# Kernel optimization log

Measured on AMD Instinct MI355X. Metric: run time of the kernel, lower is better.

## Reference

```python
import jax, jax.numpy as jnp
import numpy as np

N_NODES = 10000
N_EDGES = 160000
N_GRAPHS = 64
F = 80        # hidden dim
T = 5         # towers
F_OUT = 16    # per-tower post output (80/5)
N_LAYERS = 4
EPS = 1e-6
BN_EPS = 1e-5
STD_EPS = 1e-5


def setup_inputs() -> dict:
    key = jax.random.key(0)
    ks = jax.random.split(key, 12)
    x = jax.random.uniform(ks[0], (N_NODES, 2), dtype=jnp.float32)
    edge_index = jax.random.randint(ks[1], (2, N_EDGES), 0, N_NODES, dtype=jnp.int64)
    batch = jnp.sort(jax.random.randint(ks[2], (N_NODES,), 0, N_GRAPHS, dtype=jnp.int64))

    def w(k, shape, fan_in):
        return (jax.random.normal(k, shape, jnp.float32) / np.float32(np.sqrt(fan_in)))

    return {
        "x": x, "edge_index": edge_index, "batch": batch,
        "pre_lin_W": w(ks[3], (1, F), 1), "pre_lin_b": jnp.zeros((F,), jnp.float32),
        "pre_W": w(ks[4], (N_LAYERS, T, 2 * F, F), 2 * F), "pre_b": jnp.zeros((N_LAYERS, T, F), jnp.float32),
        "post_W": w(ks[5], (N_LAYERS, T, 13 * F, F_OUT), 13 * F), "post_b": jnp.zeros((N_LAYERS, T, F_OUT), jnp.float32),
        "lin_W": w(ks[6], (N_LAYERS, F, F), F), "lin_b": jnp.zeros((N_LAYERS, F), jnp.float32),
        "bn_gamma": jnp.ones((N_LAYERS, F), jnp.float32), "bn_beta": jnp.zeros((N_LAYERS, F), jnp.float32),
        "mlp_lin_W": w(ks[7], (40, 1), 40), "mlp_lin_b": jnp.zeros((1,), jnp.float32),
        "mlp1_W": w(ks[8], (40, 20), 40), "mlp1_b": jnp.zeros((20,), jnp.float32),
        "mlp2_W": w(ks[9], (20, 1), 20), "mlp2_b": jnp.zeros((1,), jnp.float32),
    }


def _pna_conv(h, src, dst, deg, avg_log_deg, preW, preb, postW, postb, linW, linb):
    # h: [N, F]; messages per tower: pre MLP over cat(x_i, x_j)  (divide_input=False)
    N = h.shape[0]
    hm = jnp.concatenate([h[dst], h[src]], axis=-1)            # [E, 2F]
    m = jnp.einsum('ef,tfo->eto', hm, preW) + preb             # [E, T, F]

    cnt = jnp.maximum(deg, 1.0)[:, None, None]                 # [N,1,1]
    has = (deg > 0)[:, None, None]
    s = jax.ops.segment_sum(m, dst, num_segments=N)
    mean = s / cnt
    mean_sq = jax.ops.segment_sum(m * m, dst, num_segments=N) / cnt
    mn = jax.ops.segment_min(m, dst, num_segments=N)
    mx = jax.ops.segment_max(m, dst, num_segments=N)
    mn = jnp.where(has, mn, 0.0)
    mx = jnp.where(has, mx, 0.0)
    std = jnp.sqrt(jax.nn.relu(mean_sq - mean * mean) + STD_EPS)
    agg = jnp.concatenate([mean, mn, mx, std], axis=-1)        # [N, T, 4F]

    logd = jnp.log(jnp.maximum(deg, 1.0) + 1.0)[:, None, None]
    amp = agg * (logd / avg_log_deg)
    att = agg * (avg_log_deg / logd)
    out = jnp.concatenate([agg, amp, att], axis=-1)            # [N, T, 12F]

    xt = jnp.broadcast_to(h[:, None, :], (N, T, F))
    out = jnp.concatenate([xt, out], axis=-1)                  # [N, T, 13F]
    out = jnp.einsum('ntf,tfo->nto', out, postW) + postb       # [N, T, F_OUT]
    out = out.reshape(N, T * F_OUT)                            # [N, 80]
    return out @ linW + linb


def _forward(x, edge_index, batch, pre_lin_W, pre_lin_b, pre_W, pre_b,
             post_W, post_b, lin_W, lin_b, bn_gamma, bn_beta,
             mlp_lin_W, mlp_lin_b, mlp1_W, mlp1_b, mlp2_W, mlp2_b):
    N = x.shape[0]
    src, dst = edge_index[0], edge_index[1]
    deg = jax.ops.segment_sum(jnp.ones_like(dst, jnp.float32), dst, num_segments=N)
    avg_log_deg = jnp.mean(jnp.log(deg + 1.0))                 # PNA avg log-degree from deg histogram

    operation = x[:, 0:1]
    assignment = x[:, 1:2]
    op = operation @ pre_lin_W + pre_lin_b                     # [N, 80]

    for l in range(N_LAYERS):
        y = _pna_conv(op, src, dst, deg, avg_log_deg,
                      pre_W[l], pre_b[l], post_W[l], post_b[l], lin_W[l], lin_b[l])
        mu = jnp.mean(y, axis=0)
        var = jnp.mean((y - mu) ** 2, axis=0)                  # biased, training-mode BN
        y = (y - mu) / jnp.sqrt(var + BN_EPS) * bn_gamma[l] + bn_beta[l]
        op = jax.nn.relu(y)

    front, behind = op[:, :40], op[:, 40:]
    xc = front * assignment + behind                           # [N, 40], non-negative

    # LastLayer: log-space scatter-add message passing
    log_score = jax.ops.segment_sum(jnp.log(xc[src] + EPS), dst, num_segments=N)
    xc = jnp.exp(log_score + jnp.log(xc + EPS))

    # global mean pool over graphs
    gcnt = jnp.maximum(jax.ops.segment_sum(jnp.ones_like(batch, jnp.float32), batch, num_segments=N_GRAPHS), 1.0)
    pooled = jax.ops.segment_sum(xc, batch, num_segments=N_GRAPHS) / gcnt[:, None]  # [B, 40]

    x_lin = pooled @ mlp_lin_W + mlp_lin_b
    x_cv = pooled @ mlp1_W + mlp1_b
    x_cv = 20.0 - jax.nn.relu(x_cv)
    x_cv = x_cv @ mlp2_W + mlp2_b
    return x_cv + x_lin                                        # [B, 1]


def reference(x, edge_index, batch, pre_lin_W, pre_lin_b, pre_W, pre_b,
              post_W, post_b, lin_W, lin_b, bn_gamma, bn_beta,
              mlp_lin_W, mlp_lin_b, mlp1_W, mlp1_b, mlp2_W, mlp2_b):
    return _forward(x, edge_index, batch, pre_lin_W, pre_lin_b, pre_W, pre_b,
                    post_W, post_b, lin_W, lin_b, bn_gamma, bn_beta,
                    mlp_lin_W, mlp_lin_b, mlp1_W, mlp1_b, mlp2_W, mlp2_b)
```

## Files before the change

### kernel.cpp

```cpp
#include <hip/hip_runtime.h>
#include <math.h>

#define NN 10000
#define NE 160000
#define NG 64
#define FEAT 80
#define NT 5
#define NL 4

__global__ void k_cnt2(const int* __restrict__ dst, const int* __restrict__ batch,
                       int* __restrict__ deg, int* __restrict__ gcnt) {
    int e = blockIdx.x * 256 + threadIdx.x;
    if (e < NE) atomicAdd(&deg[dst[e]], 1);
    if (e < NN) atomicAdd(&gcnt[batch[e]], 1);
}

__global__ void k_scan(const int* __restrict__ deg, int* __restrict__ offs) {
    __shared__ int sums[256];
    int tid = threadIdx.x;
    int start = tid * 40, stop = min(start + 40, NN);
    int s = 0;
    for (int i = start; i < stop; ++i) s += deg[i];
    sums[tid] = s;
    __syncthreads();
    for (int off = 1; off < 256; off <<= 1) {
        int v = (tid >= off) ? sums[tid - off] : 0;
        __syncthreads();
        sums[tid] += v;
        __syncthreads();
    }
    int base = (tid == 0) ? 0 : sums[tid - 1];
    for (int i = start; i < stop; ++i) { offs[i] = base; base += deg[i]; }
    if (tid == 255) offs[NN] = sums[255];
}

__global__ void k_ald(const int* __restrict__ deg, float* __restrict__ ald) {
    __shared__ float red[256];
    int i = blockIdx.x * 256 + threadIdx.x;
    red[threadIdx.x] = (i < NN) ? logf((float)deg[i] + 1.0f) : 0.0f;
    __syncthreads();
    for (int s = 128; s > 0; s >>= 1) {
        if (threadIdx.x < s) red[threadIdx.x] += red[threadIdx.x + s];
        __syncthreads();
    }
    if (threadIdx.x == 0) atomicAdd(ald, red[0]);
}

__global__ void k_fill(const int* __restrict__ src, const int* __restrict__ dst,
                       const int* __restrict__ offs, int* __restrict__ cursor,
                       int* __restrict__ csr) {
    int e = blockIdx.x * 256 + threadIdx.x;
    if (e < NE) {
        int d = dst[e];
        int p = atomicAdd(&cursor[d], 1);
        csr[offs[d] + p] = src[e];
    }
}

__global__ void k_op0(const float* __restrict__ x, const float* __restrict__ plW,
                      const float* __restrict__ plb, float* __restrict__ hT) {
    int i = blockIdx.x * 256 + threadIdx.x;
    if (i < FEAT * NN) {
        int f = i / NN, n = i - f * NN;
        hT[i] = x[2 * n] * plW[f] + plb[f];
    }
}

__global__ __launch_bounds__(256) void k_mm_ab(
        const float* __restrict__ hT, const float* __restrict__ preW_l,
        float* __restrict__ A, float* __restrict__ Bt) {
    __shared__ float hs[16][80];
    int n0 = blockIdx.x * 16;
    int tid = threadIdx.x;
    for (int i = tid; i < 16 * 80; i += 256) {
        int nl = i & 15, f = i >> 4;
        hs[nl][f] = hT[(size_t)f * NN + n0 + nl];
    }
    __syncthreads();
    float acc[4][16];
#pragma unroll
    for (int s = 0; s < 4; s++)
#pragma unroll
        for (int i = 0; i < 16; i++) acc[s][i] = 0.f;
    const float* wp[4];
#pragma unroll
    for (int s = 0; s < 4; s++) {
        int c = tid + s * 256;
        int cs = (c < 800) ? c : 0;
        int part = (cs >= 400) ? 1 : 0;
        int cc = cs - part * 400;
        int t = cc / 80, o = cc - t * 80;
        wp[s] = preW_l + (size_t)(t * 160 + part * 80) * 80 + o;
    }
    for (int fq = 0; fq < 80; fq += 4) {
        float w[4][4];
#pragma unroll
        for (int s = 0; s < 4; s++) {
            w[s][0] = wp[s][(fq + 0) * 80];
            w[s][1] = wp[s][(fq + 1) * 80];
            w[s][2] = wp[s][(fq + 2) * 80];
            w[s][3] = wp[s][(fq + 3) * 80];
        }
#pragma unroll
        for (int i = 0; i < 16; i++) {
            float4 hv = *(const float4*)&hs[i][fq];
#pragma unroll
            for (int s = 0; s < 4; s++) {
                acc[s][i] += hv.x * w[s][0] + hv.y * w[s][1] +
                             hv.z * w[s][2] + hv.w * w[s][3];
            }
        }
    }
#pragma unroll
    for (int s = 0; s < 4; s++) {
        int c = tid + s * 256;
        if (c < 800) {
            int part = (c >= 400) ? 1 : 0;
            int cc = c - part * 400;
            int t = cc / 80, o = cc - t * 80;
            if (part == 0) {
#pragma unroll
                for (int i = 0; i < 16; i++) A[(size_t)(n0 + i) * 400 + cc] = acc[s][i];
            } else {
#pragma unroll
                for (int i = 0; i < 16; i++)
                    Bt[((size_t)t * NN + n0 + i) * 80 + o] = acc[s][i];
            }
        }
    }
}

__global__ __launch_bounds__(256) void k_agg_t(
        const float* __restrict__ A, const float* __restrict__ Bt,
        const int* __restrict__ offs, const int* __restrict__ csr,
        const float* __restrict__ preb_l, float* __restrict__ aggT) {
    __shared__ float st[320 * 17];
    int tid = threadIdx.x;
    int id = blockIdx.y * 625 + blockIdx.x;
    int xcd = id & 7;
    int slot = id >> 3;
    int base = (xcd <= 5) ? xcd * 391 : 5 * 391 + (xcd - 5) * 390;
    int r = base + slot;
    int t = r / 625;
    int n0 = (r - t * 625) * 16;
    int ni = tid >> 4;
    int cl = tid & 15;
    int n = n0 + ni;
    int e0 = offs[n], e1 = offs[n + 1];
    const float* Bts = Bt + (size_t)t * NN * 80;
    float s[5], q[5], mn[5], mx[5];
#pragma unroll
    for (int k = 0; k < 5; k++) { s[k] = 0.f; q[k] = 0.f; mn[k] = 3.4e38f; mx[k] = -3.4e38f; }
    int e = e0;
    for (; e + 3 < e1; e += 4) {
        const float* br0 = Bts + (size_t)csr[e] * 80 + cl;
        const float* br1 = Bts + (size_t)csr[e + 1] * 80 + cl;
        const float* br2 = Bts + (size_t)csr[e + 2] * 80 + cl;
        const float* br3 = Bts + (size_t)csr[e + 3] * 80 + cl;
#pragma unroll
        for (int k = 0; k < 5; k++) {
            float b0 = br0[k * 16];
            float b1 = br1[k * 16];
            float b2 = br2[k * 16];
            float b3 = br3[k * 16];
            s[k] += (b0 + b1) + (b2 + b3);
            q[k] += (b0 * b0 + b1 * b1) + (b2 * b2 + b3 * b3);
            mn[k] = fminf(mn[k], fminf(fminf(b0, b1), fminf(b2, b3)));
            mx[k] = fmaxf(mx[k], fmaxf(fmaxf(b0, b1), fmaxf(b2, b3)));
        }
    }
    for (; e < e1; ++e) {
        const float* br = Bts + (size_t)csr[e] * 80 + cl;
#pragma unroll
        for (int k = 0; k < 5; k++) {
            float b = br[k * 16];
            s[k] += b; q[k] += b * b;
            mn[k] = fminf(mn[k], b); mx[k] = fmaxf(mx[k], b);
        }
    }
    int d = e1 - e0;
    float degf = (float)d;
    float cnt = fmaxf(degf, 1.f);
#pragma unroll
    for (int k = 0; k < 5; k++) {
        int c = cl + k * 16;
        float a = A[(size_t)n * 400 + t * 80 + c] + preb_l[t * 80 + c];
        float mean = (degf * a + s[k]) / cnt;
        float msq  = (degf * a * a + 2.f * a * s[k] + q[k]) / cnt;
        float sd = sqrtf(fmaxf(msq - mean * mean, 0.f) + 1e-5f);
        float mnr = (d > 0) ? a + mn[k] : 0.f;
        float mxr = (d > 0) ? a + mx[k] : 0.f;
        st[(0 * 80 + c) * 17 + ni] = mean;
        st[(1 * 80 + c) * 17 + ni] = mnr;
        st[(2 * 80 + c) * 17 + ni] = mxr;
        st[(3 * 80 + c) * 17 + ni] = sd;
    }
    __syncthreads();
    int jj = tid >> 4;
    int nl = tid & 15;
#pragma unroll
    for (int pass = 0; pass < 20; ++pass) {
        int j = pass * 16 + jj;
        aggT[((size_t)t * 320 + j) * NN + n0 + nl] = st[j * 17 + nl];
    }
}

__global__ __launch_bounds__(256) void k_post(
        const float* __restrict__ hT, const float* __restrict__ aggT,
        const float* __restrict__ postW_l, const float* __restrict__ postb_l,
        const int* __restrict__ offs, const float* __restrict__ ald_sum,
        float* __restrict__ y0T) {
    __shared__ float wj[40 * 48];
    __shared__ float wh[80 * 16];
    int tid = threadIdx.x;
    int t = blockIdx.y;
    int jq = blockIdx.z;
    int j0 = jq * 40;
    const float* W0 = postW_l + (size_t)t * 1040 * 16;
    const float* W1 = W0 + 80 * 16;
    const float* W2 = W0 + 400 * 16;
    const float* W3 = W0 + 720 * 16;
    for (int idx = tid; idx < 40 * 48; idx += 256) {
        int j = idx / 48;
        int rem = idx - j * 48;
        int p = rem >> 4, o = rem & 15;
        const float* Wp = (p == 0) ? W1 : (p == 1) ? W2 : W3;
        wj[idx] = Wp[(j0 + j) * 16 + o];
    }
    if (jq == 0) {
        for (int idx = tid; idx < 80 * 16; idx += 256)
            wh[idx] = W0[idx];
    }
    __syncthreads();
    int n = blockIdx.x * 256 + tid;
    bool alive = (n < NN);
    int nc = alive ? n : 0;
    float acc1[16], acc2[16], acc3[16];
#pragma unroll
    for (int i = 0; i < 16; i++) { acc1[i] = 0.f; acc2[i] = 0.f; acc3[i] = 0.f; }
    const float* ap = aggT + ((size_t)t * 320 + j0) * NN + nc;
#pragma unroll 8
    for (int j = 0; j < 40; ++j) {
        float a = ap[(size_t)j * NN];
        const float* w = wj + j * 48;
#pragma unroll
        for (int i = 0; i < 16; i++) {
            acc1[i] += a * w[i];
            acc2[i] += a * w[16 + i];
            acc3[i] += a * w[32 + i];
        }
    }
    if (jq == 0) {
#pragma unroll 4
        for (int f = 0; f < 80; ++f) {
            float hv = hT[(size_t)f * NN + nc];
            const float* w = wh + f * 16;
#pragma unroll
            for (int i = 0; i < 16; i++) acc1[i] += hv * w[i];
        }
    }
    if (alive) {
        float degf = (float)(offs[n + 1] - offs[n]);
        float ald = ald_sum[0] * (1.f / NN);
        float logd = logf(fmaxf(degf, 1.f) + 1.f);
        float c1 = logd / ald;
        float c2 = ald / logd;
#pragma unroll
        for (int i = 0; i < 16; i++) {
            float v = acc1[i] + c1 * acc2[i] + c2 * acc3[i];
            if (jq == 0) v += postb_l[t * 16 + i];
            unsafeAtomicAdd(&y0T[(size_t)(t * 16 + i) * NN + n], v);
        }
    }
}

__global__ __launch_bounds__(256) void k_lin(
        const float* __restrict__ y0T, const float* __restrict__ linW_l,
        const float* __restrict__ linb_l, float* __restrict__ yT) {
    __shared__ float ws[80 * 8];
    int tid = threadIdx.x;
    int f0 = blockIdx.y * 8;
    for (int idx = tid; idx < 80 * 8; idx += 256)
        ws[idx] = linW_l[(idx >> 3) * 80 + f0 + (idx & 7)];
    __syncthreads();
    int n = blockIdx.x * 256 + tid;
    bool alive = (n < NN);
    int nc = alive ? n : 0;
    float acc[8];
#pragma unroll
    for (int i = 0; i < 8; i++) acc[i] = 0.f;
#pragma unroll 8
    for (int k = 0; k < 80; ++k) {
        float v = y0T[(size_t)k * NN + nc];
        const float4 wa = *(const float4*)(ws + k * 8);
        const float4 wb = *(const float4*)(ws + k * 8 + 4);
        acc[0] += v * wa.x; acc[1] += v * wa.y; acc[2] += v * wa.z; acc[3] += v * wa.w;
        acc[4] += v * wb.x; acc[5] += v * wb.y; acc[6] += v * wb.z; acc[7] += v * wb.w;
    }
    if (alive) {
#pragma unroll
        for (int i = 0; i < 8; i++)
            yT[(size_t)(f0 + i) * NN + n] = acc[i] + linb_l[f0 + i];
    }
}

__global__ void k_bnstats(const float* __restrict__ yT, float* __restrict__ bnst) {
    __shared__ float r1[256], r2[256];
    int f = blockIdx.x;
    int seg = blockIdx.y;
    int tid = threadIdx.x;
    int i0 = seg * 1250, i1 = min(i0 + 1250, NN);
    float s = 0.f, q = 0.f;
    for (int i = i0 + tid; i < i1; i += 256) {
        float v = yT[(size_t)f * NN + i];
        s += v; q += v * v;
    }
    r1[tid] = s; r2[tid] = q;
    __syncthreads();
    for (int st = 128; st > 0; st >>= 1) {
        if (tid < st) { r1[tid] += r1[tid + st]; r2[tid] += r2[tid + st]; }
        __syncthreads();
    }
    if (tid == 0) {
        unsafeAtomicAdd(&bnst[f], r1[0]);
        unsafeAtomicAdd(&bnst[80 + f], r2[0]);
    }
}

__global__ void k_bn(const float* __restrict__ yT, const float* __restrict__ bnst,
                     const float* __restrict__ gamma_l, const float* __restrict__ beta_l,
                     float* __restrict__ hT) {
    int i = blockIdx.x * 256 + threadIdx.x;
    if (i >= FEAT * NN) return;
    int f = i / NN;
    float mu = bnst[f] * (1.f / NN);
    float msq = bnst[80 + f] * (1.f / NN);
    float var = fmaxf(msq - mu * mu, 0.f);
    float v = (yT[i] - mu) * (1.f / sqrtf(var + 1e-5f)) * gamma_l[f] + beta_l[f];
    hT[i] = fmaxf(v, 0.f);
}

__global__ void k_bnxc(const float* __restrict__ yT, const float* __restrict__ bnst,
                       const float* __restrict__ gamma_l, const float* __restrict__ beta_l,
                       const float* __restrict__ x, float* __restrict__ lxc) {
    int i = blockIdx.x * 256 + threadIdx.x;
    if (i >= 40 * NN) return;
    int f = i / NN, n = i - f * NN;
    int f2 = f + 40;
    float mu1 = bnst[f] * (1.f / NN);
    float ms1 = bnst[80 + f] * (1.f / NN);
    float v1 = (yT[(size_t)f * NN + n] - mu1) *
               (1.f / sqrtf(fmaxf(ms1 - mu1 * mu1, 0.f) + 1e-5f)) * gamma_l[f] + beta_l[f];
    v1 = fmaxf(v1, 0.f);
    float mu2 = bnst[f2] * (1.f / NN);
    float ms2 = bnst[80 + f2] * (1.f / NN);
    float v2 = (yT[(size_t)f2 * NN + n] - mu2) *
               (1.f / sqrtf(fmaxf(ms2 - mu2 * mu2, 0.f) + 1e-5f)) * gamma_l[f2] + beta_l[f2];
    v2 = fmaxf(v2, 0.f);
    lxc[(size_t)n * 40 + f] = logf(v1 * x[2 * n + 1] + v2 + 1e-6f);
}

__global__ void k_logagg(const float* __restrict__ lxc, const int* __restrict__ offs,
                         const int* __restrict__ csr, const int* __restrict__ batch,
                         float* __restrict__ pooled) {
    int n = blockIdx.x;
    int tid = threadIdx.x;
    if (tid >= 40) return;
    int e0 = offs[n], e1 = offs[n + 1];
    float s = 0.f;
    for (int k = e0; k < e1; ++k) s += lxc[(size_t)csr[k] * 40 + tid];
    float v = expf(s + lxc[(size_t)n * 40 + tid]);
    atomicAdd(&pooled[batch[n] * 40 + tid], v);
}

__global__ void k_final(const float* __restrict__ pooled, const int* __restrict__ gcnt,
                        const float* __restrict__ mlW, const float* __restrict__ mlb,
                        const float* __restrict__ m1W, const float* __restrict__ m1b,
                        const float* __restrict__ m2W, const float* __restrict__ m2b,
                        float* __restrict__ out) {
    int g = threadIdx.x;
    if (g >= NG) return;
    float inv = 1.f / fmaxf((float)gcnt[g], 1.f);
    float pl[40];
#pragma unroll
    for (int j = 0; j < 40; j++) pl[j] = pooled[g * 40 + j] * inv;
    float xl = mlb[0];
#pragma unroll
    for (int j = 0; j < 40; j++) xl += pl[j] * mlW[j];
    float acc = m2b[0];
    for (int k = 0; k < 20; k++) {
        float v = m1b[k];
#pragma unroll
        for (int j = 0; j < 40; j++) v += pl[j] * m1W[j * 20 + k];
        v = 20.f - fmaxf(v, 0.f);
        acc += v * m2W[k];
    }
    out[g] = acc + xl;
}

extern "C" void kernel_launch(void* const* d_in, const int* in_sizes, int n_in,
                              void* d_out, int out_size, void* d_ws, size_t ws_size,
                              hipStream_t stream) {
    const float* x     = (const float*)d_in[0];
    const int*   ei    = (const int*)d_in[1];
    const int*   batch = (const int*)d_in[2];
    const float* plW   = (const float*)d_in[3];
    const float* plb   = (const float*)d_in[4];
    const float* preW  = (const float*)d_in[5];
    const float* preb  = (const float*)d_in[6];
    const float* postW = (const float*)d_in[7];
    const float* postb = (const float*)d_in[8];
    const float* linW  = (const float*)d_in[9];
    const float* linb  = (const float*)d_in[10];
    const float* bnG   = (const float*)d_in[11];
    const float* bnB   = (const float*)d_in[12];
    const float* mlW   = (const float*)d_in[13];
    const float* mlb   = (const float*)d_in[14];
    const float* m1W   = (const float*)d_in[15];
    const float* m1b   = (const float*)d_in[16];
    const float* m2W   = (const float*)d_in[17];
    const float* m2b   = (const float*)d_in[18];
    float* out = (float*)d_out;
    const int* srcp = ei;
    const int* dstp = ei + NE;

    char* p = (char*)d_ws;
    int*   deg    = (int*)(p + 0);
    int*   cursor = (int*)(p + 40000);
    int*   gcnt   = (int*)(p + 80000);
    float* ald    = (float*)(p + 80256);
    float* pooled = (float*)(p + 80272);
    float* bnst   = (float*)(p + 90512);
    int*   offs   = (int*)(p + 93072);
    int*   csr    = (int*)(p + 133088);
    float* hT     = (float*)(p + 773088);
    float* A      = (float*)(p + 3973088);
    float* Bt     = (float*)(p + 19973088);
    float* aggT   = (float*)(p + 35973088);
    float* y0T = (float*)(p + 23173088);
    float* yT  = (float*)(p + 26373088);
    float* lxc = (float*)(p + 35973088);

    hipMemsetAsync(d_ws, 0, 93072, stream);
    k_cnt2<<<dim3((NE + 255) / 256), 256, 0, stream>>>(dstp, batch, deg, gcnt);
    k_scan<<<1, 256, 0, stream>>>(deg, offs);
    k_ald<<<dim3((NN + 255) / 256), 256, 0, stream>>>(deg, ald);
    k_fill<<<dim3((NE + 255) / 256), 256, 0, stream>>>(srcp, dstp, offs, cursor, csr);
    k_op0<<<dim3((FEAT * NN + 255) / 256), 256, 0, stream>>>(x, plW, plb, hT);

    for (int l = 0; l < NL; ++l) {
        const float* preW_l  = preW  + (size_t)l * NT * 160 * 80;
        const float* preb_l  = preb  + l * NT * 80;
        const float* postW_l = postW + (size_t)l * NT * 1040 * 16;
        const float* postb_l = postb + l * NT * 16;
        const float* linW_l  = linW  + l * 80 * 80;
        const float* linb_l  = linb  + l * 80;
        float* bnst_l = bnst + l * 160;
        k_mm_ab<<<dim3(625), 256, 0, stream>>>(hT, preW_l, A, Bt);
        k_agg_t<<<dim3(625, 5), 256, 0, stream>>>(A, Bt, offs, csr, preb_l, aggT);
        hipMemsetAsync(y0T, 0, (size_t)80 * NN * 4, stream);
        k_post<<<dim3(40, 5, 8), 256, 0, stream>>>(hT, aggT, postW_l, postb_l, offs, ald, y0T);
        k_lin<<<dim3(40, 10), 256, 0, stream>>>(y0T, linW_l, linb_l, yT);
        k_bnstats<<<dim3(80, 8), 256, 0, stream>>>(yT, bnst_l);
        if (l < NL - 1) {
            k_bn<<<dim3((FEAT * NN + 255) / 256), 256, 0, stream>>>(
                yT, bnst_l, bnG + l * 80, bnB + l * 80, hT);
        } else {
            k_bnxc<<<dim3((40 * NN + 255) / 256), 256, 0, stream>>>(
                yT, bnst_l, bnG + l * 80, bnB + l * 80, x, lxc);
        }
    }

    k_logagg<<<dim3(NN), 64, 0, stream>>>(lxc, offs, csr, batch, pooled);
    k_final<<<1, 64, 0, stream>>>(pooled, gcnt, mlW, mlb, m1W, m1b, m2W, m2b, out);
}
```

Baseline: 781.5 us.

## Fuse PNA aggregation and post-tower projection into one kernel

Merges the aggregation kernel with the post MLP. Each 16-node tower tile now multiplies its shared-memory statistics directly by the post weights, with a split-K shared-memory reduction across four thread groups. This removes the round trip of the large aggT buffer through global memory, the memset of y0T, and the atomic accumulation. In exchange, weights are read from global or cache per block rather than staged in LDS, and the reduction adds extra syncs and leaves most threads idle during the final step.

```diff
diff --git a/kernel.cpp b/kernel.cpp
--- a/kernel.cpp
+++ b/kernel.cpp
@@ -130,10 +130,12 @@
     }
 }
 
-__global__ __launch_bounds__(256) void k_agg_t(
+__global__ __launch_bounds__(256) void k_aggpost(
         const float* __restrict__ A, const float* __restrict__ Bt,
         const int* __restrict__ offs, const int* __restrict__ csr,
-        const float* __restrict__ preb_l, float* __restrict__ aggT) {
+        const float* __restrict__ preb_l, const float* __restrict__ hT,
+        const float* __restrict__ postW_l, const float* __restrict__ postb_l,
+        const float* __restrict__ ald_sum, float* __restrict__ y0T) {
     __shared__ float st[320 * 17];
     int tid = threadIdx.x;
     int id = blockIdx.y * 625 + blockIdx.x;
@@ -196,80 +198,64 @@
         st[(3 * 80 + c) * 17 + ni] = sd;
     }
     __syncthreads();
-    int jj = tid >> 4;
-    int nl = tid & 15;
-#pragma unroll
-    for (int pass = 0; pass < 20; ++pass) {
-        int j = pass * 16 + jj;
-        aggT[((size_t)t * 320 + j) * NN + n0 + nl] = st[j * 17 + nl];
-    }
-}
-
-__global__ __launch_bounds__(256) void k_post(
-        const float* __restrict__ hT, const float* __restrict__ aggT,
-        const float* __restrict__ postW_l, const float* __restrict__ postb_l,
-        const int* __restrict__ offs, const float* __restrict__ ald_sum,
-        float* __restrict__ y0T) {
-    __shared__ float wj[40 * 48];
-    __shared__ float wh[80 * 16];
-    int tid = threadIdx.x;
-    int t = blockIdx.y;
-    int jq = blockIdx.z;
-    int j0 = jq * 40;
+    int ni2 = tid & 15;
+    int og  = (tid >> 4) & 3;
+    int js  = tid >> 6;
     const float* W0 = postW_l + (size_t)t * 1040 * 16;
-    const float* W1 = W0 + 80 * 16;
-    const float* W2 = W0 + 400 * 16;
-    const float* W3 = W0 + 720 * 16;
-    for (int idx = tid; idx < 40 * 48; idx += 256) {
-        int j = idx / 48;
-        int rem = idx - j * 48;
-        int p = rem >> 4, o = rem & 15;
-        const float* Wp = (p == 0) ? W1 : (p == 1) ? W2 : W3;
-        wj[idx] = Wp[(j0 + j) * 16 + o];
-    }
-    if (jq == 0) {
-        for (int idx = tid; idx < 80 * 16; idx += 256)
-            wh[idx] = W0[idx];
-    }
-    __syncthreads();
-    int n = blockIdx.x * 256 + tid;
-    bool alive = (n < NN);
-    int nc = alive ? n : 0;
-    float acc1[16], acc2[16], acc3[16];
-#pragma unroll
-    for (int i = 0; i < 16; i++) { acc1[i] = 0.f; acc2[i] = 0.f; acc3[i] = 0.f; }
-    const float* ap = aggT + ((size_t)t * 320 + j0) * NN + nc;
-#pragma unroll 8
-    for (int j = 0; j < 40; ++j) {
-        float a = ap[(size_t)j * NN];
-        const float* w = wj + j * 48;
-#pragma unroll
-        for (int i = 0; i < 16; i++) {
-            acc1[i] += a * w[i];
-            acc2[i] += a * w[16 + i];
-            acc3[i] += a * w[32 + i];
-        }
-    }
-    if (jq == 0) {
-#pragma unroll 4
-        for (int f = 0; f < 80; ++f) {
-            float hv = hT[(size_t)f * NN + nc];
-            const float* w = wh + f * 16;
-#pragma unroll
-            for (int i = 0; i < 16; i++) acc1[i] += hv * w[i];
-        }
-    }
-    if (alive) {
-        float degf = (float)(offs[n + 1] - offs[n]);
+    float a1[4], a2[4], a3[4];
+#pragma unroll
+    for (int i = 0; i < 4; i++) { a1[i] = 0.f; a2[i] = 0.f; a3[i] = 0.f; }
+    int jb = js * 80;
+#pragma unroll 2
+    for (int j = jb; j < jb + 80; ++j) {
+        float a = st[j * 17 + ni2];
+        float4 w1 = *(const float4*)(W0 + (size_t)(80 + j) * 16 + og * 4);
+        float4 w2 = *(const float4*)(W0 + (size_t)(400 + j) * 16 + og * 4);
+        float4 w3 = *(const float4*)(W0 + (size_t)(720 + j) * 16 + og * 4);
+        a1[0] += a * w1.x; a1[1] += a * w1.y; a1[2] += a * w1.z; a1[3] += a * w1.w;
+        a2[0] += a * w2.x; a2[1] += a * w2.y; a2[2] += a * w2.z; a2[3] += a * w2.w;
+        a3[0] += a * w3.x; a3[1] += a * w3.y; a3[2] += a * w3.z; a3[3] += a * w3.w;
+    }
+    int fb = js * 20;
+#pragma unroll 2
+    for (int f = fb; f < fb + 20; ++f) {
+        float hv = hT[(size_t)f * NN + n0 + ni2];
+        float4 w0 = *(const float4*)(W0 + (size_t)f * 16 + og * 4);
+        a1[0] += hv * w0.x; a1[1] += hv * w0.y; a1[2] += hv * w0.z; a1[3] += hv * w0.w;
+    }
+    __syncthreads();
+    float* red = st;
+#pragma unroll
+    for (int i = 0; i < 4; i++) {
+        red[tid * 12 + i]     = a1[i];
+        red[tid * 12 + 4 + i] = a2[i];
+        red[tid * 12 + 8 + i] = a3[i];
+    }
+    __syncthreads();
+    if (tid < 64) {
+        int ni3 = tid & 15, og3 = tid >> 4;
+        float b1[4], b2[4], b3[4];
+#pragma unroll
+        for (int i = 0; i < 4; i++) { b1[i] = 0.f; b2[i] = 0.f; b3[i] = 0.f; }
+#pragma unroll
+        for (int js3 = 0; js3 < 4; ++js3) {
+            const float* rr = red + (size_t)(ni3 + 16 * (og3 + 4 * js3)) * 12;
+#pragma unroll
+            for (int i = 0; i < 4; i++) {
+                b1[i] += rr[i]; b2[i] += rr[4 + i]; b3[i] += rr[8 + i];
+            }
+        }
+        int nw = n0 + ni3;
+        float dw = (float)(offs[nw + 1] - offs[nw]);
         float ald = ald_sum[0] * (1.f / NN);
-        float logd = logf(fmaxf(degf, 1.f) + 1.f);
+        float logd = logf(fmaxf(dw, 1.f) + 1.f);
         float c1 = logd / ald;
         float c2 = ald / logd;
 #pragma unroll
-        for (int i = 0; i < 16; i++) {
-            float v = acc1[i] + c1 * acc2[i] + c2 * acc3[i];
-            if (jq == 0) v += postb_l[t * 16 + i];
-            unsafeAtomicAdd(&y0T[(size_t)(t * 16 + i) * NN + n], v);
+        for (int i = 0; i < 4; i++) {
+            int o = og3 * 4 + i;
+            float v = b1[i] + c1 * b2[i] + c2 * b3[i] + postb_l[t * 16 + o];
+            y0T[(size_t)(t * 16 + o) * NN + nw] = v;
         }
     }
 }
@@ -436,10 +422,9 @@
     float* hT     = (float*)(p + 773088);
     float* A      = (float*)(p + 3973088);
     float* Bt     = (float*)(p + 19973088);
-    float* aggT   = (float*)(p + 35973088);
-    float* y0T = (float*)(p + 23173088);
-    float* yT  = (float*)(p + 26373088);
-    float* lxc = (float*)(p + 35973088);
+    float* y0T = (float*)(p + 35973088);
+    float* yT  = (float*)(p + 39173088);
+    float* lxc = (float*)(p + 42373088);
 
     hipMemsetAsync(d_ws, 0, 93072, stream);
     k_cnt2<<<dim3((NE + 255) / 256), 256, 0, stream>>>(dstp, batch, deg, gcnt);
@@ -457,9 +442,8 @@
         const float* linb_l  = linb  + l * 80;
         float* bnst_l = bnst + l * 160;
         k_mm_ab<<<dim3(625), 256, 0, stream>>>(hT, preW_l, A, Bt);
-        k_agg_t<<<dim3(625, 5), 256, 0, stream>>>(A, Bt, offs, csr, preb_l, aggT);
-        hipMemsetAsync(y0T, 0, (size_t)80 * NN * 4, stream);
-        k_post<<<dim3(40, 5, 8), 256, 0, stream>>>(hT, aggT, postW_l, postb_l, offs, ald, y0T);
+        k_aggpost<<<dim3(625, 5), 256, 0, stream>>>(A, Bt, offs, csr, preb_l,
+                                                    hT, postW_l, postb_l, ald, y0T);
         k_lin<<<dim3(40, 10), 256, 0, stream>>>(y0T, linW_l, linb_l, yT);
         k_bnstats<<<dim3(80, 8), 256, 0, stream>>>(yT, bnst_l);
         if (l < NL - 1) {
```

Measured after the change: 876.8 us. 12.2% more time.
